# Performance work log

Hardware: AMD Instinct MI355X
Metric: run time of the kernel (lower is better)

The kernel has to match this reference:

```python
import jax, jax.numpy as jnp
import numpy as np

HID = 256
SLOTS = 64
K = 2
TAU = 8.0
EPS = 1e-5


def setup_inputs() -> dict:
    key = jax.random.key(0)
    ks = jax.random.split(key, 8)
    B, T = 512, 256
    s = lambda fan_in: 1.0 / np.sqrt(fan_in)
    return {
        "x": jax.random.uniform(ks[0], (B, T, 1), jnp.float32, 0.0, 10.0),
        "W_embed": jax.random.uniform(ks[1], (HID, 1), jnp.float32, -1.0, 1.0),
        "b_embed": jax.random.uniform(ks[2], (HID,), jnp.float32, -1.0, 1.0),
        "W_update": jax.random.uniform(ks[3], (HID, HID), jnp.float32, -s(HID), s(HID)),
        "b_update": jax.random.uniform(ks[4], (HID,), jnp.float32, -s(HID), s(HID)),
        "gamma": jnp.ones((HID,), jnp.float32),
        "beta": jnp.zeros((HID,), jnp.float32),
        "W_out": jax.random.uniform(ks[5], (10, HID), jnp.float32, -s(HID), s(HID)),
        "b_out": jax.random.uniform(ks[6], (10,), jnp.float32, -s(HID), s(HID)),
        "context_strength": jnp.float32(0.2),
    }


def _gaussian_attention(pointer, num_positions):
    # pointer: [B] float. Returns indices [B,5] int32, weights [B,5] float.
    offsets = jnp.arange(-K, K + 1)
    base = jnp.clip(jnp.floor(pointer).astype(jnp.int32), 0, num_positions - 1)
    indices = (base[:, None] + offsets[None, :]) % num_positions
    delta = indices.astype(pointer.dtype) - pointer[:, None]
    weights = jax.nn.softmax(-(delta ** 2) / TAU, axis=1)
    return indices, weights


def reference(x, W_embed, b_embed, W_update, b_update, gamma, beta, W_out, b_out, context_strength):
    B, T, _ = x.shape
    cs = jax.nn.sigmoid(context_strength)

    def step(carry, x_t):
        h, memory, pointer = carry  # [B,H], [B,SLOTS,H], [B]
        inp = jnp.tanh(x_t @ W_embed.T + b_embed)           # [B,H]
        indices, weights = _gaussian_attention(pointer, SLOTS)
        neighborhood = jnp.take_along_axis(memory, indices[:, :, None], axis=1)  # [B,5,H]
        context = jnp.einsum('bk,bkh->bh', weights, neighborhood)
        combined = inp + cs * context
        h = jnp.tanh((combined + h) @ W_update.T + b_update)
        mu = jnp.mean(h, axis=-1, keepdims=True)
        var = jnp.mean((h - mu) ** 2, axis=-1, keepdims=True)
        h = (h - mu) * jax.lax.rsqrt(var + EPS) * gamma + beta
        contribution = weights[:, :, None] * h[:, None, :]   # [B,5,H]
        memory = jax.vmap(lambda m, i, c: m.at[i].add(c))(memory, indices, contribution)
        pointer = (pointer + 1.0) % SLOTS
        return (h, memory, pointer), None

    h0 = jnp.zeros((B, HID), x.dtype)
    mem0 = jnp.zeros((B, SLOTS, HID), x.dtype)
    ptr0 = jnp.zeros((B,), x.dtype)
    (h, _, _), _ = jax.lax.scan(step, (h0, mem0, ptr0), jnp.swapaxes(x, 0, 1))
    return h @ W_out.T + b_out
```

## Files before the change

kernel.cpp:

```cpp
#include <hip/hip_runtime.h>


#define TT 256

typedef __bf16 bf16x8 __attribute__((ext_vector_type(8)));
typedef float  f32x4  __attribute__((ext_vector_type(4)));
typedef float  f32x2  __attribute__((ext_vector_type(2)));

#define C2 2.8853900817779268f

__device__ __forceinline__ float tanh_pre(float u) {
    float e = exp2f(u);
    return 1.f - __fdividef(2.f, e + 1.f);
}

template<int CTRL, int RM>
__device__ __forceinline__ float dpp_add(float v) {
    int t = __builtin_amdgcn_update_dpp(0, __float_as_int(v), CTRL, RM, 0xf, true);
    return v + __int_as_float(t);
}
__device__ __forceinline__ float dpp_xor2_mov(float v) {
    int t = __builtin_amdgcn_update_dpp(0, __float_as_int(v), 0x4E, 0xf, 0xf, true);
    return __int_as_float(t);
}
__device__ __forceinline__ float swap32_add(float v) {
    float a = v, b = v;
    asm("v_permlane32_swap_b32 %0, %1" : "+v"(a), "+v"(b));
    return a + b;
}
__device__ __forceinline__ float swap16_add(float v) {
    float a = v, b = v;
    asm("v_permlane16_swap_b32 %0, %1" : "+v"(a), "+v"(b));
    return a + b;
}

#define SMEM_BYTES 136432

__global__ __launch_bounds__(512, 2)
void postnorm_kernel(const float* __restrict__ x,
                     const float* __restrict__ W_embed,
                     const float* __restrict__ b_embed,
                     const float* __restrict__ W_update,
                     const float* __restrict__ b_update,
                     const float* __restrict__ gamma,
                     const float* __restrict__ beta,
                     const float* __restrict__ W_out,
                     const float* __restrict__ b_out,
                     const float* __restrict__ ctx_s,
                     float* __restrict__ out)
{
    extern __shared__ __align__(16) char smem[];
    float*  s_mem  = (float*)(smem);
    float*  s_x    = (float*)(smem + 131072);
    __bf16* s_v    = (__bf16*)(smem + 133120);
    float*  s_acc  = (float*)(smem + 134272);
    float*  s_wt   = (float*)(smem + 134304);
    float*  s_oacc = (float*)(smem + 136352);

    const int tid  = threadIdx.x;
    const int wave = tid >> 6;
    const int lane = tid & 63;
    const int bn   = lane & 15;
    const int quad = lane >> 4;
    const int r0   = blockIdx.x * 2;

    const int b     = bn >> 1;
    const int row   = bn & 1;
    const int i_own = wave * 32 + (b >> 2) * 16 + quad * 4 + (b & 3);

    {   f32x4 z = {0.f, 0.f, 0.f, 0.f};
        f32x4* p = (f32x4*)s_mem;
        #pragma unroll
        for (int k = 0; k < 16; ++k) p[tid + k * 512] = z;
    }
    s_x[tid] = x[(r0 + (tid >> 8)) * TT + (tid & 255)];
    if (tid < 8)  s_acc[tid] = 0.f;
    if (tid < 20) s_oacc[tid] = 0.f;

    if (tid < 64) {
        float wv[5]; float ssum = 0.f;
        #pragma unroll
        for (int k = 0; k < 5; ++k) {
            int idx = (tid + k - 2) & 63;
            float d = (float)idx - (float)tid;
            wv[k] = expf(-(d * d) * 0.125f);
            ssum += wv[k];
        }
        #pragma unroll
        for (int k = 0; k < 5; ++k) s_wt[tid * 8 + k] = wv[k] / ssum;
    }

    const float csv = 1.f / (1.f + expf(-ctx_s[0]));

    const float we2 = W_embed[i_own] * C2;
    const float be2 = b_embed[i_own] * C2;
    const float gm  = gamma[i_own];
    const float btt = beta[i_own];

    f32x4 bu4a = *(const f32x4*)(b_update + wave * 32 + quad * 4);
    f32x4 bu4b = *(const f32x4*)(b_update + wave * 32 + 16 + quad * 4);
    #pragma unroll
    for (int j = 0; j < 4; ++j) { bu4a[j] *= C2; bu4b[j] *= C2; }

    bf16x8 wfa[2][8];
    #pragma unroll
    for (int mt = 0; mt < 2; ++mt) {
        #pragma unroll
        for (int kt = 0; kt < 8; ++kt) {
            const float* wp = W_update + (wave * 32 + mt * 16 + bn) * 256
                                       + kt * 32 + quad * 8;
            f32x4 a = *(const f32x4*)wp;
            f32x4 bb = *(const f32x4*)(wp + 4);
            bf16x8 f;
            f[0] = (__bf16)(a[0] * C2);  f[1] = (__bf16)(a[1] * C2);
            f[2] = (__bf16)(a[2] * C2);  f[3] = (__bf16)(a[3] * C2);
            f[4] = (__bf16)(bb[0] * C2); f[5] = (__bf16)(bb[1] * C2);
            f[6] = (__bf16)(bb[2] * C2); f[7] = (__bf16)(bb[3] * C2);
            wfa[mt][kt] = f;
        }
    }

    __syncthreads();
    {
        float inp0 = tanh_pre(fmaf(s_x[row * 256], we2, be2));
        s_v[row * 288 + i_own] = (__bf16)inp0;
    }

    float wt0, wt1, wt2, wt3, wt4;
    {   f32x4 wv = *(const f32x4*)(s_wt);
        wt0 = wv[0]; wt1 = wv[1]; wt2 = wv[2]; wt3 = wv[3]; wt4 = s_wt[4];
    }
    f32x4 nw  = *(const f32x4*)(s_wt + 8);
    float nw4 = s_wt[8 + 4];
    float xn  = s_x[row * 256 + 1];
    float nf  = 0.f;
    __syncthreads();

    float hn = 0.f;
    float w0 = 0.f, w1 = 0.f, w2 = 0.f, w3 = 0.f, w4 = 0.f;
    float* mcol = s_mem + (row << 14) + i_own;
    const __bf16* vsrc = s_v + row * 288 + quad * 8;

    #pragma unroll 1
    for (int t = 0; t < TT; ++t) {
        const int rb = t & 1, wb = rb ^ 1;

        float inp  = tanh_pre(fmaf(xn, we2, be2));
        float ctxA = ((nw[0] * w1 + nw[1] * w2) + (nw[2] * w3 + nw[3] * w4))
                   + nw4 * nf;
        float wdot = (nw[0] * wt1 + nw[1] * wt2) + (nw[2] * wt3 + nw[3] * wt4);
        float base = fmaf(csv, ctxA, inp);
        float coef = fmaf(csv, wdot, 1.f);

        f32x4 a0a = bu4a, a1a = bu4b;
        f32x4 a0b = {0,0,0,0}, a1b = {0,0,0,0};
        #pragma unroll
        for (int kt = 0; kt < 4; ++kt) {
            bf16x8 bfr0 = *(const bf16x8*)(vsrc + kt * 32);
            bf16x8 bfr1 = *(const bf16x8*)(vsrc + (kt + 4) * 32);
            a0a = __builtin_amdgcn_mfma_f32_16x16x32_bf16(wfa[0][kt],     bfr0, a0a, 0, 0, 0);
            a1a = __builtin_amdgcn_mfma_f32_16x16x32_bf16(wfa[1][kt],     bfr0, a1a, 0, 0, 0);
            a0b = __builtin_amdgcn_mfma_f32_16x16x32_bf16(wfa[0][kt + 4], bfr1, a0b, 0, 0, 0);
            a1b = __builtin_amdgcn_mfma_f32_16x16x32_bf16(wfa[1][kt + 4], bfr1, a1b, 0, 0, 0);
        }

        f32x4 y0 = a0a + a0b, y1 = a1a + a1b;
        f32x4 ym = (b & 4) ? y1 : y0;
        float yA = (b & 2) ? ym[2] : ym[0];
        float yB = (b & 2) ? ym[3] : ym[1];
        float ysel = (b & 1) ? yB : yA;

        float yt = tanh_pre(ysel);
        float e  = dpp_xor2_mov(yt);
        float v0 = yt + e;
        float v1 = fmaf(e, e, yt * yt);
        float s  = ((lane >> 1) & 1) ? v1 : v0;
        s = dpp_add<0x124, 0xf>(s);
        s = dpp_add<0x128, 0xf>(s);
        s = swap16_add(s);
        s = swap32_add(s);
        if (lane < 4)
            atomicAdd(&s_acc[rb * 4 + (lane & 1) * 2 + (lane >> 1)], s);
        __syncthreads();

        f32x2 S = *(const f32x2*)(s_acc + rb * 4 + row * 2);
        if (tid < 4) s_acc[wb * 4 + tid] = 0.f;
        float mu   = S[0] * (1.f / 256.f);
        float var  = S[1] * (1.f / 256.f) - mu * mu;
        float rstd = rsqrtf(var + 1e-5f);
        hn = fmaf(yt - mu, rstd * gm, btt);
        float v = fmaf(coef, hn, base);
        s_v[row * 288 + i_own] = (__bf16)v;

        float rv = fmaf(wt0, hn, w0);
        w0 = fmaf(wt1, hn, w1); w1 = fmaf(wt2, hn, w2);
        w2 = fmaf(wt3, hn, w3); w3 = fmaf(wt4, hn, w4); w4 = nf;
        mcol[((t - 2) & 63) << 8] = rv;
        wt0 = nw[0]; wt1 = nw[1]; wt2 = nw[2]; wt3 = nw[3]; wt4 = nw4;
        nf  = mcol[((t + 4) & 63) << 8];
        {   const float* wp = s_wt + ((t + 2) & 63) * 8;
            nw  = *(const f32x4*)wp;
            nw4 = wp[4];
        }
        xn  = s_x[row * 256 + ((t + 2) & 255)];
        __syncthreads();
    }

    s_x[row * 256 + i_own] = hn;
    __syncthreads();
    {
        const int n = tid >> 8, i = tid & 255;
        float h = s_x[tid];
        #pragma unroll
        for (int o = 0; o < 10; ++o) {
            float p = h * W_out[o * 256 + i];
            #pragma unroll
            for (int m = 32; m >= 1; m >>= 1) p += __shfl_xor(p, m, 64);
            if (lane == 0) atomicAdd(&s_oacc[n * 10 + o], p);
        }
    }
    __syncthreads();
    if (tid < 20) {
        int nn = tid / 10, o = tid % 10;
        out[(r0 + nn) * 10 + o] = s_oacc[tid] + b_out[o];
    }
}

extern "C" void kernel_launch(void* const* d_in, const int* in_sizes, int n_in,
                              void* d_out, int out_size, void* d_ws, size_t ws_size,
                              hipStream_t stream) {
    const float* x    = (const float*)d_in[0];
    const float* W_e  = (const float*)d_in[1];
    const float* b_e  = (const float*)d_in[2];
    const float* W_u  = (const float*)d_in[3];
    const float* b_u  = (const float*)d_in[4];
    const float* gmm  = (const float*)d_in[5];
    const float* bta  = (const float*)d_in[6];
    const float* W_o  = (const float*)d_in[7];
    const float* b_o  = (const float*)d_in[8];
    const float* cst  = (const float*)d_in[9];
    float* out = (float*)d_out;

    (void)hipFuncSetAttribute(reinterpret_cast<const void*>(postnorm_kernel),
                              hipFuncAttributeMaxDynamicSharedMemorySize,
                              SMEM_BYTES);

    postnorm_kernel<<<dim3(256), dim3(512), SMEM_BYTES, stream>>>(
        x, W_e, b_e, W_u, b_u, gmm, bta, W_o, b_o, cst, out);
}
```

Measured before the change: 287.4 us.

## Fold LayerNorm into next-step matmul to remove one barrier per step

Restructures the recurrence so the LayerNorm of step t is applied algebraically after the next matmul. The unnormalised tanh output and the context input are fed as separate MFMA operand columns, and the mean and rstd are combined afterwards with a precomputed W·gamma term. Per-wave partial sums go to a double-buffered reduction array instead of shared atomics, which removes the second __syncthreads per timestep. In exchange the MFMA B operand doubles in width, there is extra bf16 rounding on gamma*yt, and the memory-update pipeline gets longer.

```diff
diff --git a/kernel.cpp b/kernel.cpp
--- a/kernel.cpp
+++ b/kernel.cpp
@@ -34,7 +34,7 @@
     return a + b;
 }
 
-#define SMEM_BYTES 136432
+#define SMEM_BYTES 139856
 
 __global__ __launch_bounds__(512, 2)
 void postnorm_kernel(const float* __restrict__ x,
@@ -53,9 +53,9 @@
     float*  s_mem  = (float*)(smem);
     float*  s_x    = (float*)(smem + 131072);
     __bf16* s_v    = (__bf16*)(smem + 133120);
-    float*  s_acc  = (float*)(smem + 134272);
-    float*  s_wt   = (float*)(smem + 134304);
-    float*  s_oacc = (float*)(smem + 136352);
+    float*  s_red  = (float*)(smem + 137472);
+    float*  s_wt   = (float*)(smem + 137728);
+    float*  s_oacc = (float*)(smem + 139776);
 
     const int tid  = threadIdx.x;
     const int wave = tid >> 6;
@@ -64,9 +64,12 @@
     const int quad = lane >> 4;
     const int r0   = blockIdx.x * 2;
 
-    const int b     = bn >> 1;
-    const int row   = bn & 1;
-    const int i_own = wave * 32 + (b >> 2) * 16 + quad * 4 + (b & 3);
+    const int row  = bn & 1;
+    const int pq   = (bn >> 1) & 1;
+    const int rep  = bn >> 2;
+    const int mt   = rep >> 1;
+    const int rsel = (rep & 1) * 2 + pq;
+    const int i_own = wave * 32 + mt * 16 + quad * 4 + rsel;
 
     {   f32x4 z = {0.f, 0.f, 0.f, 0.f};
         f32x4* p = (f32x4*)s_mem;
@@ -74,23 +77,31 @@
         for (int k = 0; k < 16; ++k) p[tid + k * 512] = z;
     }
     s_x[tid] = x[(r0 + (tid >> 8)) * TT + (tid & 255)];
-    if (tid < 8)  s_acc[tid] = 0.f;
+    if (tid < 64) s_red[tid] = 0.f;
     if (tid < 20) s_oacc[tid] = 0.f;
 
+    const float csv = 1.f / (1.f + expf(-ctx_s[0]));
+
     if (tid < 64) {
-        float wv[5]; float ssum = 0.f;
+        float wv[5], wp[5]; float sa = 0.f, sb = 0.f;
+        const int pm = (tid + 63) & 63;
         #pragma unroll
         for (int k = 0; k < 5; ++k) {
-            int idx = (tid + k - 2) & 63;
-            float d = (float)idx - (float)tid;
-            wv[k] = expf(-(d * d) * 0.125f);
-            ssum += wv[k];
-        }
-        #pragma unroll
-        for (int k = 0; k < 5; ++k) s_wt[tid * 8 + k] = wv[k] / ssum;
-    }
-
-    const float csv = 1.f / (1.f + expf(-ctx_s[0]));
+            int ia = (tid + k - 2) & 63;
+            float da = (float)ia - (float)tid;
+            wv[k] = expf(-(da * da) * 0.125f);  sa += wv[k];
+            int ib = (pm + k - 2) & 63;
+            float db = (float)ib - (float)pm;
+            wp[k] = expf(-(db * db) * 0.125f);  sb += wp[k];
+        }
+        float ra = 1.f / sa, rb2 = 1.f / sb;
+        #pragma unroll
+        for (int k = 0; k < 5; ++k) { wv[k] *= ra; wp[k] *= rb2; }
+        #pragma unroll
+        for (int k = 0; k < 5; ++k) s_wt[tid * 8 + k] = wv[k];
+        float cd = (wv[0] * wp[1] + wv[1] * wp[2]) + (wv[2] * wp[3] + wv[3] * wp[4]);
+        s_wt[tid * 8 + 5] = fmaf(csv, cd, 1.f);
+    }
 
     const float we2 = W_embed[i_own] * C2;
     const float be2 = b_embed[i_own] * C2;
@@ -99,78 +110,120 @@
 
     f32x4 bu4a = *(const f32x4*)(b_update + wave * 32 + quad * 4);
     f32x4 bu4b = *(const f32x4*)(b_update + wave * 32 + 16 + quad * 4);
+    const f32x4 z4 = {0.f, 0.f, 0.f, 0.f};
+    f32x4 cinA, cinB;
     #pragma unroll
-    for (int j = 0; j < 4; ++j) { bu4a[j] *= C2; bu4b[j] *= C2; }
+    for (int j = 0; j < 4; ++j) {
+        cinA[j] = pq ? 0.f : bu4a[j] * C2;
+        cinB[j] = pq ? 0.f : bu4b[j] * C2;
+    }
 
     bf16x8 wfa[2][8];
     #pragma unroll
-    for (int mt = 0; mt < 2; ++mt) {
+    for (int m = 0; m < 2; ++m) {
         #pragma unroll
         for (int kt = 0; kt < 8; ++kt) {
-            const float* wp = W_update + (wave * 32 + mt * 16 + bn) * 256
-                                       + kt * 32 + quad * 8;
-            f32x4 a = *(const f32x4*)wp;
-            f32x4 bb = *(const f32x4*)(wp + 4);
+            const float* wpp = W_update + (wave * 32 + m * 16 + bn) * 256
+                                        + kt * 32 + quad * 8;
+            f32x4 a = *(const f32x4*)wpp;
+            f32x4 bb = *(const f32x4*)(wpp + 4);
             bf16x8 f;
             f[0] = (__bf16)(a[0] * C2);  f[1] = (__bf16)(a[1] * C2);
             f[2] = (__bf16)(a[2] * C2);  f[3] = (__bf16)(a[3] * C2);
             f[4] = (__bf16)(bb[0] * C2); f[5] = (__bf16)(bb[1] * C2);
             f[6] = (__bf16)(bb[2] * C2); f[7] = (__bf16)(bb[3] * C2);
-            wfa[mt][kt] = f;
-        }
-    }
-
-    __syncthreads();
+            wfa[m][kt] = f;
+        }
+    }
+
+    s_v[row * 272 + i_own]       = (__bf16)gm;
+    s_v[(row + 2) * 272 + i_own] = (__bf16)gm;
+    __syncthreads();
+    float yG2;
+    {
+        const __bf16* vs0 = s_v + (bn & 3) * 272 + quad * 8;
+        f32x4 a0a = z4, a0b = z4, a1a = z4, a1b = z4;
+        #pragma unroll
+        for (int kt = 0; kt < 4; ++kt) {
+            bf16x8 b0 = *(const bf16x8*)(vs0 + kt * 32);
+            bf16x8 b1 = *(const bf16x8*)(vs0 + (kt + 4) * 32);
+            a0a = __builtin_amdgcn_mfma_f32_16x16x32_bf16(wfa[0][kt],     b0, a0a, 0, 0, 0);
+            a1a = __builtin_amdgcn_mfma_f32_16x16x32_bf16(wfa[1][kt],     b0, a1a, 0, 0, 0);
+            a0b = __builtin_amdgcn_mfma_f32_16x16x32_bf16(wfa[0][kt + 4], b1, a0b, 0, 0, 0);
+            a1b = __builtin_amdgcn_mfma_f32_16x16x32_bf16(wfa[1][kt + 4], b1, a1b, 0, 0, 0);
+        }
+        f32x4 y0 = a0a + a0b, y1 = a1a + a1b;
+        f32x4 ym = mt ? y1 : y0;
+        float pl = (rep & 1) ? ym[2] : ym[0];
+        float ph = (rep & 1) ? ym[3] : ym[1];
+        yG2 = pq ? ph : pl;
+    }
+    __syncthreads();
+
     {
         float inp0 = tanh_pre(fmaf(s_x[row * 256], we2, be2));
-        s_v[row * 288 + i_own] = (__bf16)inp0;
-    }
-
-    float wt0, wt1, wt2, wt3, wt4;
-    {   f32x4 wv = *(const f32x4*)(s_wt);
-        wt0 = wv[0]; wt1 = wv[1]; wt2 = wv[2]; wt3 = wv[3]; wt4 = s_wt[4];
-    }
-    f32x4 nw  = *(const f32x4*)(s_wt + 8);
-    float nw4 = s_wt[8 + 4];
-    float xn  = s_x[row * 256 + 1];
-    float nf  = 0.f;
-    __syncthreads();
-
-    float hn = 0.f;
-    float w0 = 0.f, w1 = 0.f, w2 = 0.f, w3 = 0.f, w4 = 0.f;
+        s_v[row * 272 + i_own]       = (__bf16)inp0;
+        s_v[(row + 2) * 272 + i_own] = (__bf16)0.f;
+    }
+    float u0 = 0.f, u1 = 0.f, u2 = 0.f, u3 = 0.f, u4 = 0.f, u5 = 0.f;
+    float yt_prev = 0.f, Ccur = 1.f;
+    float nf = 0.f;
+    float xn = s_x[row * 256 + 1];
     float* mcol = s_mem + (row << 14) + i_own;
-    const __bf16* vsrc = s_v + row * 288 + quad * 8;
+    __syncthreads();
 
     #pragma unroll 1
     for (int t = 0; t < TT; ++t) {
         const int rb = t & 1, wb = rb ^ 1;
-
-        float inp  = tanh_pre(fmaf(xn, we2, be2));
-        float ctxA = ((nw[0] * w1 + nw[1] * w2) + (nw[2] * w3 + nw[3] * w4))
-                   + nw4 * nf;
-        float wdot = (nw[0] * wt1 + nw[1] * wt2) + (nw[2] * wt3 + nw[3] * wt4);
-        float base = fmaf(csv, ctxA, inp);
-        float coef = fmaf(csv, wdot, 1.f);
-
-        f32x4 a0a = bu4a, a1a = bu4b;
-        f32x4 a0b = {0,0,0,0}, a1b = {0,0,0,0};
+        const float m0 = (t == 0) ? 0.f : 1.f;
+
+        const float* rp = s_red + wb * 32;
+        f32x4 p1a = *(const f32x4*)(rp + row * 8);
+        f32x4 p1b = *(const f32x4*)(rp + row * 8 + 4);
+        f32x4 p2a = *(const f32x4*)(rp + (2 + row) * 8);
+        f32x4 p2b = *(const f32x4*)(rp + (2 + row) * 8 + 4);
+        const float* wrN = s_wt + ((t + 1) & 63) * 8;
+        f32x4 nww = *(const f32x4*)wrN;
+        f32x2 nwc = *(const f32x2*)(wrN + 4);
+        const float* wrM = s_wt + ((t + 63) & 63) * 8;
+        f32x4 mww = *(const f32x4*)wrM;
+        float mw4 = wrM[4];
+        float inp = tanh_pre(fmaf(xn, we2, be2));
+
+        const __bf16* vsrc = s_v + (rb * 4 + (bn & 3)) * 272 + quad * 8;
+        f32x4 a0a = cinA, a1a = cinB, a0b = z4, a1b = z4;
         #pragma unroll
         for (int kt = 0; kt < 4; ++kt) {
-            bf16x8 bfr0 = *(const bf16x8*)(vsrc + kt * 32);
-            bf16x8 bfr1 = *(const bf16x8*)(vsrc + (kt + 4) * 32);
-            a0a = __builtin_amdgcn_mfma_f32_16x16x32_bf16(wfa[0][kt],     bfr0, a0a, 0, 0, 0);
-            a1a = __builtin_amdgcn_mfma_f32_16x16x32_bf16(wfa[1][kt],     bfr0, a1a, 0, 0, 0);
-            a0b = __builtin_amdgcn_mfma_f32_16x16x32_bf16(wfa[0][kt + 4], bfr1, a0b, 0, 0, 0);
-            a1b = __builtin_amdgcn_mfma_f32_16x16x32_bf16(wfa[1][kt + 4], bfr1, a1b, 0, 0, 0);
-        }
+            bf16x8 b0 = *(const bf16x8*)(vsrc + kt * 32);
+            bf16x8 b1 = *(const bf16x8*)(vsrc + (kt + 4) * 32);
+            a0a = __builtin_amdgcn_mfma_f32_16x16x32_bf16(wfa[0][kt],     b0, a0a, 0, 0, 0);
+            a1a = __builtin_amdgcn_mfma_f32_16x16x32_bf16(wfa[1][kt],     b0, a1a, 0, 0, 0);
+            a0b = __builtin_amdgcn_mfma_f32_16x16x32_bf16(wfa[0][kt + 4], b1, a0b, 0, 0, 0);
+            a1b = __builtin_amdgcn_mfma_f32_16x16x32_bf16(wfa[1][kt + 4], b1, a1b, 0, 0, 0);
+        }
+
+        float S1 = ((p1a[0] + p1a[1]) + (p1a[2] + p1a[3]))
+                 + ((p1b[0] + p1b[1]) + (p1b[2] + p1b[3]));
+        float S2 = ((p2a[0] + p2a[1]) + (p2a[2] + p2a[3]))
+                 + ((p2b[0] + p2b[1]) + (p2b[2] + p2b[3]));
+        float mu   = S1 * (1.f / 256.f);
+        float var  = S2 * (1.f / 256.f) - mu * mu;
+        float rstd = rsqrtf(var + 1e-5f);
+        float aC = rstd * Ccur * m0;
+        float bC = -mu * aC;
 
         f32x4 y0 = a0a + a0b, y1 = a1a + a1b;
-        f32x4 ym = (b & 4) ? y1 : y0;
-        float yA = (b & 2) ? ym[2] : ym[0];
-        float yB = (b & 2) ? ym[3] : ym[1];
-        float ysel = (b & 1) ? yB : yA;
-
-        float yt = tanh_pre(ysel);
+        f32x4 ym = mt ? y1 : y0;
+        float pl = (rep & 1) ? ym[2] : ym[0];
+        float ph = (rep & 1) ? ym[3] : ym[1];
+        float own  = pq ? ph : pl;
+        float give = pq ? pl : ph;
+        float recv = dpp_xor2_mov(give);
+        float yP = pq ? recv : own;
+        float yQ = pq ? own  : recv;
+        float u  = fmaf(bC, yG2, fmaf(aC, yQ, yP));
+        float yt = tanh_pre(u);
+
         float e  = dpp_xor2_mov(yt);
         float v0 = yt + e;
         float v1 = fmaf(e, e, yt * yt);
@@ -179,34 +232,45 @@
         s = dpp_add<0x128, 0xf>(s);
         s = swap16_add(s);
         s = swap32_add(s);
-        if (lane < 4)
-            atomicAdd(&s_acc[rb * 4 + (lane & 1) * 2 + (lane >> 1)], s);
+        if (lane < 4) s_red[rb * 32 + lane * 8 + wave] = s;
+
+        float hn = m0 * fmaf(yt_prev - mu, rstd * gm, btt);
+        u0 = fmaf(mww[0], hn, u0); u1 = fmaf(mww[1], hn, u1);
+        u2 = fmaf(mww[2], hn, u2); u3 = fmaf(mww[3], hn, u3);
+        u4 = fmaf(mw4,    hn, u4);
+        mcol[((t + 61) & 63) << 8] = u0;
+        u0 = u1; u1 = u2; u2 = u3; u3 = u4; u4 = u5; u5 = nf;
+
+        float ctxB = ((nww[0] * u1 + nww[1] * u2) + (nww[2] * u3 + nww[3] * u4))
+                   + nwc[0] * u5;
+        float vP = fmaf(nwc[1], btt, fmaf(csv, ctxB, inp));
+        float vQ = gm * yt;
+        __bf16* svw = s_v + wb * 1088;
+        svw[row * 272 + i_own]       = (__bf16)vP;
+        svw[(row + 2) * 272 + i_own] = (__bf16)vQ;
+
+        Ccur = nwc[1];  yt_prev = yt;
+        nf = mcol[((t + 4) & 63) << 8];
+        xn = s_x[row * 256 + ((t + 2) & 255)];
         __syncthreads();
-
-        f32x2 S = *(const f32x2*)(s_acc + rb * 4 + row * 2);
-        if (tid < 4) s_acc[wb * 4 + tid] = 0.f;
-        float mu   = S[0] * (1.f / 256.f);
-        float var  = S[1] * (1.f / 256.f) - mu * mu;
+    }
+
+    {
+        const float* rp = s_red + 1 * 32;
+        f32x4 p1a = *(const f32x4*)(rp + row * 8);
+        f32x4 p1b = *(const f32x4*)(rp + row * 8 + 4);
+        f32x4 p2a = *(const f32x4*)(rp + (2 + row) * 8);
+        f32x4 p2b = *(const f32x4*)(rp + (2 + row) * 8 + 4);
+        float S1 = ((p1a[0] + p1a[1]) + (p1a[2] + p1a[3]))
+                 + ((p1b[0] + p1b[1]) + (p1b[2] + p1b[3]));
+        float S2 = ((p2a[0] + p2a[1]) + (p2a[2] + p2a[3]))
+                 + ((p2b[0] + p2b[1]) + (p2b[2] + p2b[3]));
+        float mu   = S1 * (1.f / 256.f);
+        float var  = S2 * (1.f / 256.f) - mu * mu;
         float rstd = rsqrtf(var + 1e-5f);
-        hn = fmaf(yt - mu, rstd * gm, btt);
-        float v = fmaf(coef, hn, base);
-        s_v[row * 288 + i_own] = (__bf16)v;
-
-        float rv = fmaf(wt0, hn, w0);
-        w0 = fmaf(wt1, hn, w1); w1 = fmaf(wt2, hn, w2);
-        w2 = fmaf(wt3, hn, w3); w3 = fmaf(wt4, hn, w4); w4 = nf;
-        mcol[((t - 2) & 63) << 8] = rv;
-        wt0 = nw[0]; wt1 = nw[1]; wt2 = nw[2]; wt3 = nw[3]; wt4 = nw4;
-        nf  = mcol[((t + 4) & 63) << 8];
-        {   const float* wp = s_wt + ((t + 2) & 63) * 8;
-            nw  = *(const f32x4*)wp;
-            nw4 = wp[4];
-        }
-        xn  = s_x[row * 256 + ((t + 2) & 255)];
-        __syncthreads();
-    }
-
-    s_x[row * 256 + i_own] = hn;
+        float hfin = fmaf(yt_prev - mu, rstd * gm, btt);
+        s_x[row * 256 + i_own] = hfin;
+    }
     __syncthreads();
     {
         const int n = tid >> 8, i = tid & 255;
```

Result: slower. 305.4 us (+6.3%).
